# Performance work log

Measured on AMD Instinct MI355X. Metric: run time of the kernel, lower is better.

## Reference

```python
import jax, jax.numpy as jnp
import numpy as np

D_MODEL = 1024
N_HEADS = 16
HEAD_DIM = D_MODEL // N_HEADS


def setup_inputs() -> dict:
    key = jax.random.key(0)
    kx, kq, kk, kv, ko = jax.random.split(key, 5)
    B, T = 4, 2048
    s = 1.0 / np.sqrt(D_MODEL)
    return {
        "x": jax.random.normal(kx, (B, T, D_MODEL), dtype=jnp.float32),
        "W_Q": jax.random.normal(kq, (D_MODEL, D_MODEL), dtype=jnp.float32) * s,
        "W_K": jax.random.normal(kk, (D_MODEL, D_MODEL), dtype=jnp.float32) * s,
        "W_V": jax.random.normal(kv, (D_MODEL, D_MODEL), dtype=jnp.float32) * s,
        "W_O": jax.random.normal(ko, (D_MODEL, D_MODEL), dtype=jnp.float32) * s,
    }


def reference(x, W_Q, W_K, W_V, W_O):
    B, T, C = x.shape
    H, hd = N_HEADS, HEAD_DIM
    # nn.Linear applies x @ W.T; W_* here are the [out,in] weight matrices.
    def proj(W):
        return (x @ W.T).reshape(B, T, H, hd).transpose(0, 2, 1, 3)  # [B,H,T,hd]
    q, k, v = proj(W_Q), proj(W_K), proj(W_V)
    scale = 1.0 / np.sqrt(hd).astype(np.float32)
    attn = jnp.einsum("bhqd,bhkd->bhqk", q, k) * scale  # [B,H,T,T]
    causal = jnp.tril(jnp.ones((T, T), dtype=bool))
    attn = jnp.where(causal, attn, -jnp.inf)
    attn = jax.nn.softmax(attn, axis=-1)
    out = jnp.einsum("bhqk,bhkd->bhqd", attn, v)  # [B,H,T,hd]
    out = out.transpose(0, 2, 1, 3).reshape(B, T, C)
    return out @ W_O.T
```

## Files before the change

### kernel.cpp

```cpp
#include <hip/hip_runtime.h>
#include <hip/hip_bf16.h>
#include <stdint.h>


typedef __attribute__((ext_vector_type(8))) short short8;
typedef __attribute__((ext_vector_type(4))) short short4v;
typedef __attribute__((ext_vector_type(4))) float floatx4;

#define LOG2E 1.4426950408889634f

__device__ __forceinline__ void gload_lds16(const void* g, void* l) {
  __builtin_amdgcn_global_load_lds(
      (const __attribute__((address_space(1))) void*)g,
      (__attribute__((address_space(3))) void*)l, 16, 0, 0);
}

__device__ __forceinline__ short f2bf(float f) {
  __hip_bfloat16 h = __float2bfloat16(f);
  return *reinterpret_cast<short*>(&h);
}

__global__ __launch_bounds__(256) void cvt_f32_bf16(const float* __restrict__ src,
                                                    short* __restrict__ dst, int n4,
                                                    float scale) {
  const int i = blockIdx.x * blockDim.x + threadIdx.x;
  if (i >= n4) return;
  const float4 v = reinterpret_cast<const float4*>(src)[i];
  short4v o;
  o.x = f2bf(v.x * scale); o.y = f2bf(v.y * scale);
  o.z = f2bf(v.z * scale); o.w = f2bf(v.w * scale);
  reinterpret_cast<short4v*>(dst)[i] = o;
}

__global__ __launch_bounds__(256) void cvt_weights(const float* __restrict__ wq,
                                                   const float* __restrict__ wk,
                                                   const float* __restrict__ wv,
                                                   const float* __restrict__ wo,
                                                   short* __restrict__ dst0,
                                                   float qscale) {
  const int y = blockIdx.y;
  const float* src = (y == 0) ? wq : (y == 1) ? wk : (y == 2) ? wv : wo;
  const float scale = (y == 0) ? qscale : 1.0f;
  short* dst = dst0 + (size_t)y * 1048576;
  const int i = blockIdx.x * blockDim.x + threadIdx.x;
  const float4 v = reinterpret_cast<const float4*>(src)[i];
  short4v o;
  o.x = f2bf(v.x * scale); o.y = f2bf(v.y * scale);
  o.z = f2bf(v.z * scale); o.w = f2bf(v.w * scale);
  reinterpret_cast<short4v*>(&dst[i * 4])[0] = o;
}

template <int MODE>
__device__ __forceinline__ void gemm256_body(const short* __restrict__ A,
                                             const short* __restrict__ B,
                                             void* __restrict__ Cout,
                                             int m0, int n0,
                                             short* __restrict__ la0,
                                             short* __restrict__ la1,
                                             short* __restrict__ la2,
                                             short* __restrict__ lb0,
                                             short* __restrict__ lb1,
                                             short* __restrict__ lb2) {
  const int tid = threadIdx.x;
  const int lane = tid & 63;
  const int w = tid >> 6;
  const int wm = w >> 1, wn = w & 1;
  const int lrow = lane & 15, lgrp = lane >> 4;

  floatx4 acc[4][4] = {};

  const int srow = tid >> 2;
  const int scb = (tid & 3) ^ (srow & 3) ^ ((srow & 4) >> 1);
  const short* ag = A + (size_t)(m0 + srow) * 1024 + scb * 8;
  const short* bg = B + (size_t)(n0 + srow) * 1024 + scb * 8;

  auto stage3 = [&](short* la, short* lb) {
    gload_lds16(ag, la + tid * 8);
    gload_lds16(ag + 128 * 1024, la + (512 + tid) * 8);
    gload_lds16(bg, lb + tid * 8);
    ag += 32; bg += 32;
  };

  const int slA = (lgrp ^ (lrow & 3) ^ ((lrow & 4) >> 1)) * 8;

  auto tile = [&](const short* la, const short* lb, short* na, short* nb, bool pf) {
    if (pf) stage3(na, nb);
    short8 af[4], bf[4];
#pragma unroll
    for (int mf = 0; mf < 4; ++mf) {
      const int row = wm * 64 + mf * 16 + lrow;
      af[mf] = *reinterpret_cast<const short8*>(&la[row * 32 + slA]);
    }
#pragma unroll
    for (int nf = 0; nf < 4; ++nf) {
      const int row = wn * 64 + nf * 16 + lrow;
      bf[nf] = *reinterpret_cast<const short8*>(&lb[row * 32 + slA]);
    }
    __builtin_amdgcn_s_setprio(1);
#pragma unroll
    for (int mf = 0; mf < 4; ++mf)
#pragma unroll
      for (int nf = 0; nf < 4; ++nf)
        acc[mf][nf] = __builtin_amdgcn_mfma_f32_16x16x32_bf16(af[mf], bf[nf], acc[mf][nf], 0, 0, 0);
    __builtin_amdgcn_s_setprio(0);
  };

  auto tiletop = [&](int n) {
    __builtin_amdgcn_sched_barrier(0);
    if (n == 0)
      asm volatile("s_waitcnt vmcnt(0)" ::: "memory");
    else
      asm volatile("s_waitcnt vmcnt(3)" ::: "memory");
    __builtin_amdgcn_s_barrier();
    __builtin_amdgcn_sched_barrier(0);
  };

  stage3(la0, lb0);
  stage3(la1, lb1);

#pragma unroll 1
  for (int kt = 0; kt < 30; kt += 3) {
    tiletop(3); tile(la0, lb0, la2, lb2, true);
    tiletop(3); tile(la1, lb1, la0, lb0, true);
    tiletop(3); tile(la2, lb2, la1, lb1, true);
  }
  tiletop(3); tile(la0, lb0, nullptr, nullptr, false);
  tiletop(0); tile(la1, lb1, nullptr, nullptr, false);

#pragma unroll
  for (int mf = 0; mf < 4; ++mf) {
#pragma unroll
    for (int nf = 0; nf < 4; ++nf) {
      if (MODE == 2) {
        short4v pk;
#pragma unroll
        for (int r = 0; r < 4; ++r) pk[r] = f2bf(acc[mf][nf][r]);
        const int t0 = m0 + wm * 64 + mf * 16 + lgrp * 4;
        const int ch = n0 + wn * 64 + nf * 16 + lrow;
        const int bh = ((t0 >> 11) << 4) + (ch >> 6);
        short* Vt = reinterpret_cast<short*>(Cout);
        *reinterpret_cast<short4v*>(
            &Vt[(size_t)bh * 131072 + (size_t)(ch & 63) * 2048 + (t0 & 2047)]) = pk;
      } else {
#pragma unroll
        for (int r = 0; r < 4; ++r) {
          const int grow = m0 + wm * 64 + mf * 16 + lgrp * 4 + r;
          const int gcol = n0 + wn * 64 + nf * 16 + lrow;
          if (MODE == 1)
            reinterpret_cast<short*>(Cout)[(size_t)grow * 1024 + gcol] = f2bf(acc[mf][nf][r]);
          else
            reinterpret_cast<float*>(Cout)[(size_t)grow * 1024 + gcol] = acc[mf][nf][r];
        }
      }
    }
  }
}

__global__ __launch_bounds__(512) void gemm_qkv(
    const short* __restrict__ xb, const short* __restrict__ wq, const short* __restrict__ wk,
    const short* __restrict__ wv, short* __restrict__ Qb, short* __restrict__ Kb,
    short* __restrict__ Vt) {
  __shared__ short lds_a[3][256 * 32];
  __shared__ short lds_b[3][128 * 32];
  const int flat = blockIdx.x;
  const int xcd = flat & 7, rest = flat >> 3;
  const int nblk = rest & 7, pg = rest >> 3;
  const int panel = pg * 8 + xcd;
  const int m = panel & 31, z = panel >> 5;
  const int m0 = m * 256, n0 = nblk * 128;
  if (z == 0)
    gemm256_body<1>(xb, wq, Qb, m0, n0, lds_a[0], lds_a[1], lds_a[2],
                    lds_b[0], lds_b[1], lds_b[2]);
  else if (z == 1)
    gemm256_body<1>(xb, wk, Kb, m0, n0, lds_a[0], lds_a[1], lds_a[2],
                    lds_b[0], lds_b[1], lds_b[2]);
  else
    gemm256_body<2>(xb, wv, Vt, m0, n0, lds_a[0], lds_a[1], lds_a[2],
                    lds_b[0], lds_b[1], lds_b[2]);
}

__global__ __launch_bounds__(512) void gemm_out(const short* __restrict__ Ob,
                                                const short* __restrict__ wo,
                                                float* __restrict__ out) {
  __shared__ short lds_a[3][256 * 32];
  __shared__ short lds_b[3][128 * 32];
  const int flat = blockIdx.x;
  const int xcd = flat & 7, rest = flat >> 3;
  const int nblk = rest & 7, pg = rest >> 3;
  const int panel = pg * 8 + xcd;
  gemm256_body<0>(Ob, wo, out, panel * 256, nblk * 128,
                  lds_a[0], lds_a[1], lds_a[2], lds_b[0], lds_b[1], lds_b[2]);
}

__global__ __launch_bounds__(256, 2) void attn_fwd(const short* __restrict__ Q,
                                                   const short* __restrict__ K,
                                                   const short* __restrict__ Vt,
                                                   short* __restrict__ O) {
  __shared__ short lds_k[2][64 * 64];
  __shared__ short lds_v[2][64 * 64];
  __shared__ short lds_p[4][2][16 * 64];

  const int tid = threadIdx.x;
  const int lane = tid & 63;
  const int w = tid >> 6;
  const int lrow = lane & 15, lgrp = lane >> 4;
  const int flat = blockIdx.x;
  const int bh = flat & 63;
  const int p = flat >> 6;
  const int b = bh >> 4, h = bh & 15;

  const size_t base = (size_t)b * 2048 * 1024 + h * 64;
  const size_t vbase = (size_t)bh * 131072;

  const int srow = tid >> 3;
  const int scb = (tid & 7) ^ (srow & 7);
  const size_t koff = (size_t)srow * 1024 + scb * 8;
  const size_t voff = (size_t)srow * 2048 + scb * 8;
  short* const kd0 = &lds_k[0][tid * 8];
  short* const kd1 = &lds_k[1][tid * 8];
  short* const vd0 = &lds_v[0][tid * 8];
  short* const vd1 = &lds_v[1][tid * 8];

  auto stageK = [&](short* ldst, const short* gsrc) {
    gload_lds16(gsrc, ldst);
    gload_lds16(gsrc + 32 * 1024, ldst + 2048);
  };
  auto stageV = [&](short* ldst, const short* gsrc) {
    gload_lds16(gsrc, ldst);
    gload_lds16(gsrc + 32 * 2048, ldst + 2048);
  };

#pragma unroll 1
  for (int pass = 0; pass < 2; ++pass) {
    const int qc = pass == 0 ? (15 - p) : p;
    const int qw = qc * 128 + w * 32;
    const int lastkb = 2 * qc + (w >> 1);
    const int nkb = 2 * qc + 2;

    short8 qf[2][2];
#pragma unroll
    for (int qt = 0; qt < 2; ++qt) {
      const short* qp = Q + base + (size_t)(qw + qt * 16 + lrow) * 1024 + lgrp * 8;
      qf[qt][0] = *reinterpret_cast<const short8*>(qp);
      qf[qt][1] = *reinterpret_cast<const short8*>(qp + 32);
    }

    floatx4 oacc[2][4] = {};
    float lsum0 = 0.f, lsum1 = 0.f;

    const short* kg = K + base + koff;
    const short* vg = Vt + vbase + voff;

    auto body = [&](int kb, const short* __restrict__ ldsk,
                    const short* __restrict__ ldsv) {
      if (kb > lastkb) return;
      floatx4 s[2][4];
      __builtin_amdgcn_s_setprio(1);
#pragma unroll
      for (int nf = 0; nf < 4; ++nf) {
        const short8 kf0 = *reinterpret_cast<const short8*>(
            &ldsk[(nf * 16 + lrow) * 64 + ((lgrp) ^ (lrow & 7)) * 8]);
        const short8 kf1 = *reinterpret_cast<const short8*>(
            &ldsk[(nf * 16 + lrow) * 64 + ((4 + lgrp) ^ (lrow & 7)) * 8]);
#pragma unroll
        for (int qt = 0; qt < 2; ++qt) {
          floatx4 z = {};
          z = __builtin_amdgcn_mfma_f32_16x16x32_bf16(kf0, qf[qt][0], z, 0, 0, 0);
          z = __builtin_amdgcn_mfma_f32_16x16x32_bf16(kf1, qf[qt][1], z, 0, 0, 0);
          s[qt][nf] = z;
        }
      }
      __builtin_amdgcn_s_setprio(0);

      if (kb == lastkb) {
#pragma unroll
        for (int qt = 0; qt < 2; ++qt)
#pragma unroll
          for (int nf = 0; nf < 4; ++nf)
#pragma unroll
            for (int r = 0; r < 4; ++r) {
              const int kg_ = kb * 64 + nf * 16 + lgrp * 4 + r;
              const int qg_ = qw + qt * 16 + lrow;
              if (kg_ > qg_) s[qt][nf][r] = -1e30f;
            }
      }

#pragma unroll
      for (int qt = 0; qt < 2; ++qt) {
        float ls = 0.f;
#pragma unroll
        for (int nf = 0; nf < 4; ++nf) {
          const float p0 = __builtin_amdgcn_exp2f(s[qt][nf][0]);
          const float p1 = __builtin_amdgcn_exp2f(s[qt][nf][1]);
          const float p2 = __builtin_amdgcn_exp2f(s[qt][nf][2]);
          const float p3 = __builtin_amdgcn_exp2f(s[qt][nf][3]);
          ls += (p0 + p1) + (p2 + p3);
          short4v pk;
          pk.x = f2bf(p0); pk.y = f2bf(p1); pk.z = f2bf(p2); pk.w = f2bf(p3);
          const int c8 = (nf * 4 + lgrp) ^ ((lrow & 7) << 1);
          *reinterpret_cast<short4v*>(&lds_p[w][qt][lrow * 64 + c8 * 4]) = pk;
        }
        if (qt == 0) lsum0 += ls; else lsum1 += ls;
      }

      short8 pa[2][2];
      {
        const int c0 = ((lgrp) ^ (lrow & 7)) * 8;
        const int c1 = ((4 + lgrp) ^ (lrow & 7)) * 8;
#pragma unroll
        for (int qt = 0; qt < 2; ++qt) {
          pa[qt][0] = *reinterpret_cast<const short8*>(&lds_p[w][qt][lrow * 64 + c0]);
          pa[qt][1] = *reinterpret_cast<const short8*>(&lds_p[w][qt][lrow * 64 + c1]);
        }
      }
      __builtin_amdgcn_s_setprio(1);
#pragma unroll
      for (int nf = 0; nf < 4; ++nf) {
        const short8 vf0 = *reinterpret_cast<const short8*>(
            &ldsv[(nf * 16 + lrow) * 64 + ((lgrp) ^ (lrow & 7)) * 8]);
        const short8 vf1 = *reinterpret_cast<const short8*>(
            &ldsv[(nf * 16 + lrow) * 64 + ((4 + lgrp) ^ (lrow & 7)) * 8]);
#pragma unroll
        for (int qt = 0; qt < 2; ++qt) {
          oacc[qt][nf] = __builtin_amdgcn_mfma_f32_16x16x32_bf16(pa[qt][0], vf0, oacc[qt][nf], 0, 0, 0);
          oacc[qt][nf] = __builtin_amdgcn_mfma_f32_16x16x32_bf16(pa[qt][1], vf1, oacc[qt][nf], 0, 0, 0);
        }
      }
      __builtin_amdgcn_s_setprio(0);
    };

    stageK(kd0, kg); kg += 65536;
    stageV(vd0, vg); vg += 64;
    __syncthreads();

#pragma unroll 1
    for (int kb = 0; kb < nkb; kb += 2) {
      if (kb + 1 < nkb) { stageK(kd1, kg); kg += 65536; stageV(vd1, vg); vg += 64; }
      body(kb, lds_k[0], lds_v[0]);
      __syncthreads();
      if (kb + 1 >= nkb) break;
      if (kb + 2 < nkb) { stageK(kd0, kg); kg += 65536; stageV(vd0, vg); vg += 64; }
      body(kb + 1, lds_k[1], lds_v[1]);
      __syncthreads();
    }

    lsum0 += __shfl_xor(lsum0, 16, 64);
    lsum0 += __shfl_xor(lsum0, 32, 64);
    lsum1 += __shfl_xor(lsum1, 16, 64);
    lsum1 += __shfl_xor(lsum1, 32, 64);
#pragma unroll
    for (int qt = 0; qt < 2; ++qt) {
      const float lw = qt == 0 ? lsum0 : lsum1;
#pragma unroll
      for (int r = 0; r < 4; ++r) {
        const float linv = 1.0f / __shfl(lw, lgrp * 4 + r, 64);
        const int t = qw + qt * 16 + lgrp * 4 + r;
#pragma unroll
        for (int nf = 0; nf < 4; ++nf)
          O[base + (size_t)t * 1024 + nf * 16 + lrow] = f2bf(oacc[qt][nf][r] * linv);
      }
    }
  }
}

extern "C" void kernel_launch(void* const* d_in, const int* in_sizes, int n_in,
                              void* d_out, int out_size, void* d_ws, size_t ws_size,
                              hipStream_t stream) {
  const float* x  = (const float*)d_in[0];
  const float* Wq = (const float*)d_in[1];
  const float* Wk = (const float*)d_in[2];
  const float* Wv = (const float*)d_in[3];
  const float* Wo = (const float*)d_in[4];

  uint8_t* ws = (uint8_t*)d_ws;
  short* xb  = (short*)(ws + 0);
  short* wqb = (short*)(ws + 16777216);
  short* wkb = (short*)(ws + 18874368);
  short* wvb = (short*)(ws + 20971520);
  short* wob = (short*)(ws + 23068672);
  short* Qb  = (short*)(ws + 25165824);
  short* Kb  = (short*)(ws + 41943040);
  short* Vt  = (short*)(ws + 58720256);
  short* Ob  = (short*)(ws + 75497472);
  if (ws_size < 92274688ull) return;

  const float qscale = 0.125f * LOG2E;

  cvt_f32_bf16<<<8192, 256, 0, stream>>>(x, xb, 2097152, 1.0f);
  cvt_weights<<<dim3(1024, 4), 256, 0, stream>>>(Wq, Wk, Wv, Wo, wqb, qscale);

  gemm_qkv<<<768, 512, 0, stream>>>(xb, wqb, wkb, wvb, Qb, Kb, Vt);
  attn_fwd<<<512, 256, 0, stream>>>(Qb, Kb, Vt, Ob);
  gemm_out<<<256, 512, 0, stream>>>(Ob, wob, (float*)d_out);
}
```

Baseline: 155.4 us.

## Fuse Q/K/V projections into one GEMM block sharing the A tile

Each QKV GEMM block now computes the Q, K and V outputs for its 256x128 tile, loading each x tile into LDS once and reusing it against three weight tiles. The grid drops from 768 to 256 blocks. This cuts redundant global and LDS loads of x and the A-fragment LDS reads by a factor of three. In exchange, accumulator registers triple (48 floatx4 per thread) and LDS grows, which risks spills and lower occupancy, and the smaller grid may underfill the 256 CUs and lose the XCD-aware block swizzle.

```diff
diff --git a/kernel.cpp b/kernel.cpp
--- a/kernel.cpp
+++ b/kernel.cpp
@@ -50,6 +50,115 @@
   reinterpret_cast<short4v*>(&dst[i * 4])[0] = o;
 }
 
+__global__ __launch_bounds__(512) void gemm_qkv(
+    const short* __restrict__ xb, const short* __restrict__ wqkv,
+    short* __restrict__ Qb, short* __restrict__ Kb, short* __restrict__ Vt) {
+  __shared__ short lds_a[3][256 * 32];
+  __shared__ short lds_b[3][3 * 128 * 32];
+  const int tid = threadIdx.x;
+  const int lane = tid & 63;
+  const int w = tid >> 6;
+  const int wm = w >> 1, wn = w & 1;
+  const int lrow = lane & 15, lgrp = lane >> 4;
+
+  const int flat = blockIdx.x;
+  const int n0 = (flat & 7) * 128;
+  const int m0 = (flat >> 3) * 256;
+
+  floatx4 acc[3][4][4] = {};
+
+  const int srow = tid >> 2;
+  const int scb = (tid & 3) ^ (srow & 3) ^ ((srow & 4) >> 1);
+  const short* ag = xb + (size_t)(m0 + srow) * 1024 + scb * 8;
+  const short* bg = wqkv + (size_t)(n0 + srow) * 1024 + scb * 8;
+
+  auto stage5 = [&](short* la, short* lb) {
+    gload_lds16(ag, la + tid * 8);
+    gload_lds16(ag + 128 * 1024, la + (512 + tid) * 8);
+    gload_lds16(bg,           lb + tid * 8);
+    gload_lds16(bg + 1048576, lb + 4096 + tid * 8);
+    gload_lds16(bg + 2097152, lb + 8192 + tid * 8);
+    ag += 32; bg += 32;
+  };
+
+  const int slA = (lgrp ^ (lrow & 3) ^ ((lrow & 4) >> 1)) * 8;
+
+  auto tile = [&](const short* la, const short* lb, short* na, short* nb, bool pf) {
+    if (pf) stage5(na, nb);
+    short8 af[4];
+#pragma unroll
+    for (int mf = 0; mf < 4; ++mf)
+      af[mf] = *reinterpret_cast<const short8*>(
+          &la[(wm * 64 + mf * 16 + lrow) * 32 + slA]);
+#pragma unroll
+    for (int z = 0; z < 3; ++z) {
+      short8 bf[4];
+#pragma unroll
+      for (int nf = 0; nf < 4; ++nf)
+        bf[nf] = *reinterpret_cast<const short8*>(
+            &lb[z * 4096 + (wn * 64 + nf * 16 + lrow) * 32 + slA]);
+      __builtin_amdgcn_s_setprio(1);
+#pragma unroll
+      for (int mf = 0; mf < 4; ++mf)
+#pragma unroll
+        for (int nf = 0; nf < 4; ++nf)
+          acc[z][mf][nf] = __builtin_amdgcn_mfma_f32_16x16x32_bf16(
+              af[mf], bf[nf], acc[z][mf][nf], 0, 0, 0);
+      __builtin_amdgcn_s_setprio(0);
+    }
+  };
+
+  auto tiletop = [&](int n) {
+    __builtin_amdgcn_sched_barrier(0);
+    if (n == 0)
+      asm volatile("s_waitcnt vmcnt(0)" ::: "memory");
+    else
+      asm volatile("s_waitcnt vmcnt(5)" ::: "memory");
+    __builtin_amdgcn_s_barrier();
+    __builtin_amdgcn_sched_barrier(0);
+  };
+
+  stage5(lds_a[0], lds_b[0]);
+  stage5(lds_a[1], lds_b[1]);
+
+#pragma unroll 1
+  for (int kt = 0; kt < 30; kt += 3) {
+    tiletop(5); tile(lds_a[0], lds_b[0], lds_a[2], lds_b[2], true);
+    tiletop(5); tile(lds_a[1], lds_b[1], lds_a[0], lds_b[0], true);
+    tiletop(5); tile(lds_a[2], lds_b[2], lds_a[1], lds_b[1], true);
+  }
+  tiletop(5); tile(lds_a[0], lds_b[0], nullptr, nullptr, false);
+  tiletop(0); tile(lds_a[1], lds_b[1], nullptr, nullptr, false);
+
+#pragma unroll
+  for (int z = 0; z < 3; ++z) {
+#pragma unroll
+    for (int mf = 0; mf < 4; ++mf) {
+#pragma unroll
+      for (int nf = 0; nf < 4; ++nf) {
+        if (z == 2) {
+          short4v pk;
+#pragma unroll
+          for (int r = 0; r < 4; ++r) pk[r] = f2bf(acc[z][mf][nf][r]);
+          const int t0 = m0 + wm * 64 + mf * 16 + lgrp * 4;
+          const int ch = n0 + wn * 64 + nf * 16 + lrow;
+          const int bh = ((t0 >> 11) << 4) + (ch >> 6);
+          *reinterpret_cast<short4v*>(
+              &Vt[(size_t)bh * 131072 + (size_t)(ch & 63) * 2048 + (t0 & 2047)]) = pk;
+        } else {
+          short* C = (z == 0) ? Qb : Kb;
+#pragma unroll
+          for (int r = 0; r < 4; ++r) {
+            const int grow = m0 + wm * 64 + mf * 16 + lgrp * 4 + r;
+            const int gcol = n0 + wn * 64 + nf * 16 + lrow;
+            C[(size_t)grow * 1024 + gcol] = f2bf(acc[z][mf][nf][r]);
+          }
+        }
+      }
+    }
+  }
+}
+
 template <int MODE>
 __device__ __forceinline__ void gemm256_body(const short* __restrict__ A,
                                              const short* __restrict__ B,
@@ -131,52 +240,17 @@
   for (int mf = 0; mf < 4; ++mf) {
 #pragma unroll
     for (int nf = 0; nf < 4; ++nf) {
-      if (MODE == 2) {
-        short4v pk;
-#pragma unroll
-        for (int r = 0; r < 4; ++r) pk[r] = f2bf(acc[mf][nf][r]);
-        const int t0 = m0 + wm * 64 + mf * 16 + lgrp * 4;
-        const int ch = n0 + wn * 64 + nf * 16 + lrow;
-        const int bh = ((t0 >> 11) << 4) + (ch >> 6);
-        short* Vt = reinterpret_cast<short*>(Cout);
-        *reinterpret_cast<short4v*>(
-            &Vt[(size_t)bh * 131072 + (size_t)(ch & 63) * 2048 + (t0 & 2047)]) = pk;
-      } else {
-#pragma unroll
-        for (int r = 0; r < 4; ++r) {
-          const int grow = m0 + wm * 64 + mf * 16 + lgrp * 4 + r;
-          const int gcol = n0 + wn * 64 + nf * 16 + lrow;
-          if (MODE == 1)
-            reinterpret_cast<short*>(Cout)[(size_t)grow * 1024 + gcol] = f2bf(acc[mf][nf][r]);
-          else
-            reinterpret_cast<float*>(Cout)[(size_t)grow * 1024 + gcol] = acc[mf][nf][r];
-        }
+#pragma unroll
+      for (int r = 0; r < 4; ++r) {
+        const int grow = m0 + wm * 64 + mf * 16 + lgrp * 4 + r;
+        const int gcol = n0 + wn * 64 + nf * 16 + lrow;
+        if (MODE == 1)
+          reinterpret_cast<short*>(Cout)[(size_t)grow * 1024 + gcol] = f2bf(acc[mf][nf][r]);
+        else
+          reinterpret_cast<float*>(Cout)[(size_t)grow * 1024 + gcol] = acc[mf][nf][r];
       }
     }
   }
-}
-
-__global__ __launch_bounds__(512) void gemm_qkv(
-    const short* __restrict__ xb, const short* __restrict__ wq, const short* __restrict__ wk,
-    const short* __restrict__ wv, short* __restrict__ Qb, short* __restrict__ Kb,
-    short* __restrict__ Vt) {
-  __shared__ short lds_a[3][256 * 32];
-  __shared__ short lds_b[3][128 * 32];
-  const int flat = blockIdx.x;
-  const int xcd = flat & 7, rest = flat >> 3;
-  const int nblk = rest & 7, pg = rest >> 3;
-  const int panel = pg * 8 + xcd;
-  const int m = panel & 31, z = panel >> 5;
-  const int m0 = m * 256, n0 = nblk * 128;
-  if (z == 0)
-    gemm256_body<1>(xb, wq, Qb, m0, n0, lds_a[0], lds_a[1], lds_a[2],
-                    lds_b[0], lds_b[1], lds_b[2]);
-  else if (z == 1)
-    gemm256_body<1>(xb, wk, Kb, m0, n0, lds_a[0], lds_a[1], lds_a[2],
-                    lds_b[0], lds_b[1], lds_b[2]);
-  else
-    gemm256_body<2>(xb, wv, Vt, m0, n0, lds_a[0], lds_a[1], lds_a[2],
-                    lds_b[0], lds_b[1], lds_b[2]);
 }
 
 __global__ __launch_bounds__(512) void gemm_out(const short* __restrict__ Ob,
@@ -375,8 +449,6 @@
   uint8_t* ws = (uint8_t*)d_ws;
   short* xb  = (short*)(ws + 0);
   short* wqb = (short*)(ws + 16777216);
-  short* wkb = (short*)(ws + 18874368);
-  short* wvb = (short*)(ws + 20971520);
   short* wob = (short*)(ws + 23068672);
   short* Qb  = (short*)(ws + 25165824);
   short* Kb  = (short*)(ws + 41943040);
@@ -389,7 +461,7 @@
   cvt_f32_bf16<<<8192, 256, 0, stream>>>(x, xb, 2097152, 1.0f);
   cvt_weights<<<dim3(1024, 4), 256, 0, stream>>>(Wq, Wk, Wv, Wo, wqb, qscale);
 
-  gemm_qkv<<<768, 512, 0, stream>>>(xb, wqb, wkb, wvb, Qb, Kb, Vt);
+  gemm_qkv<<<256, 512, 0, stream>>>(xb, wqb, Qb, Kb, Vt);
   attn_fwd<<<512, 256, 0, stream>>>(Qb, Kb, Vt, Ob);
   gemm_out<<<256, 512, 0, stream>>>(Ob, wob, (float*)d_out);
 }
```

New measurement: 148.3 us. 4.6% less time.
